# Kernel tuning notes

Measured on AMD Instinct MI355X. Metric: run time of the kernel, lower is better.

Reference implementation:

```python
import jax, jax.numpy as jnp
import numpy as np
from jax.ops import segment_sum

N_NODES = 1_000_000
N_EDGES = 10_000_000


def gcn_conv(x, W, b, src, dst, n_nodes):
    """PyG GCNConv: add self-loops, sym-normalize, linear, scatter-sum, bias."""
    h = x @ W  # [N, out]
    loop = jnp.arange(n_nodes, dtype=src.dtype)
    s = jnp.concatenate([src, loop])  # sources incl. self-loops
    d = jnp.concatenate([dst, loop])  # targets incl. self-loops
    deg = segment_sum(jnp.ones(s.shape[0], dtype=h.dtype), d, num_segments=n_nodes)
    dinv = jnp.where(deg > 0, jax.lax.rsqrt(deg), 0.0)  # deg^-1/2, 0 for isolated
    norm = dinv[s] * dinv[d]  # [E+N]
    msg = h[s] * norm[:, None]  # gather + scale
    out = segment_sum(msg, d, num_segments=n_nodes)  # scatter-add at targets
    return out + b


def setup_inputs() -> dict:
    key = jax.random.key(0)
    k1, k2, k3, k4, k5 = jax.random.split(key, 5)
    x = jax.random.normal(k1, (N_NODES, 3), dtype=jnp.float32)
    edge_index = jax.random.randint(k2, (2, N_EDGES), 0, N_NODES, dtype=jnp.int64)
    # Glorot-ish init for the two GCNConv layers (3->8, 8->2) with bias
    W1 = jax.random.normal(k3, (3, 8), dtype=jnp.float32) * (1.0 / np.sqrt(3.0))
    b1 = jnp.zeros((8,), dtype=jnp.float32)
    W2 = jax.random.normal(k4, (8, 2), dtype=jnp.float32) * (1.0 / np.sqrt(8.0))
    b2 = jnp.zeros((2,), dtype=jnp.float32)
    return {"x": x, "edge_index": edge_index, "W1": W1, "b1": b1, "W2": W2, "b2": b2}


def reference(x, edge_index, W1, b1, W2, b2):
    src, dst = edge_index[0], edge_index[1]
    n = x.shape[0]
    h = gcn_conv(x, W1, b1, src, dst, n)
    h = jax.nn.relu(h)
    return gcn_conv(h, W2, b2, src, dst, n)
```

## Files before the change

kernel.cpp:

```cpp
#include <hip/hip_runtime.h>


#define BSH 12
#define BKT 4096
#define NBKT_MAX 256
#define CAP 43008
#define TILE 8192
#define MSB 512
#define AGB 512

__device__ inline unsigned bf16r(float f) {
    unsigned u = __float_as_uint(f);
    return (u + 0x7FFFu + ((u >> 16) & 1u)) & 0xFFFF0000u;
}

__device__ inline void xq_dec(unsigned u, float& v0, float& v1, float& v2) {
    float sc = __uint_as_float((((u >> 27) & 31u) + 104u) << 23);
    v0 = (float)(((int)(u << 5)) >> 23) * sc;
    v1 = (float)(((int)(u << 14)) >> 23) * sc;
    v2 = (float)(((int)(u << 23)) >> 23) * sc;
}

__global__ void k_init(int* __restrict__ bcur, int nbkt) {
    int t = threadIdx.x;
    if (t < nbkt) bcur[t] = t * CAP;
}

__global__ void k_msplit(const int* __restrict__ src, const int* __restrict__ dst,
                         int* __restrict__ bcur, unsigned* __restrict__ esort, int e) {
    __shared__ unsigned stage[TILE];
    __shared__ unsigned char bid[TILE];
    __shared__ int h[NBKT_MAX];
    __shared__ int lscan[NBKT_MAX];
    __shared__ int baseadj[NBKT_MAX];
    int t = threadIdx.x;
    int base = blockIdx.x * TILE;
    int cnt = min(TILE, e - base);
    if (t < NBKT_MAX) h[t] = 0;
    __syncthreads();

    unsigned val[16];
    int bk[16], rnk[16];
#pragma unroll
    for (int k = 0; k < 16; ++k) {
        int i = base + k * MSB + t;
        bk[k] = -1;
        if (i < e) {
            int d = __builtin_nontemporal_load(&dst[i]);
            int s = __builtin_nontemporal_load(&src[i]);
            bk[k] = d >> BSH;
            val[k] = ((unsigned)(d & (BKT - 1)) << 20) | (unsigned)s;
            rnk[k] = atomicAdd(&h[bk[k]], 1);
        }
    }
    __syncthreads();
    int c = (t < NBKT_MAX) ? h[t] : 0;
    __syncthreads();
    if (t < NBKT_MAX) lscan[t] = c;
    __syncthreads();
    for (int off = 1; off < NBKT_MAX; off <<= 1) {
        int w = (t < NBKT_MAX && t >= off) ? lscan[t - off] : 0;
        __syncthreads();
        if (t < NBKT_MAX) lscan[t] += w;
        __syncthreads();
    }
    int ex = (t < NBKT_MAX) ? (lscan[t] - c) : 0;
    __syncthreads();
    if (t < NBKT_MAX) {
        lscan[t] = ex;
        if (c > 0) baseadj[t] = atomicAdd(&bcur[t], c) - ex;
    }
    __syncthreads();

#pragma unroll
    for (int k = 0; k < 16; ++k) {
        if (bk[k] >= 0) {
            int idx = lscan[bk[k]] + rnk[k];
            stage[idx] = val[k];
            bid[idx] = (unsigned char)bk[k];
        }
    }
    __syncthreads();
#pragma unroll
    for (int k = 0; k < 16; ++k) {
        int j = k * MSB + t;
        if (j < cnt) esort[baseadj[bid[j]] + j] = stage[j];
    }
}

__global__ void k_deg_xd(const unsigned* __restrict__ esort, const int* __restrict__ bcur,
                         const float* __restrict__ x,
                         unsigned* __restrict__ xq, float* __restrict__ dinv, int n) {
    __shared__ int deg[BKT];
    int b = blockIdx.x, t = threadIdx.x;
#pragma unroll
    for (int k = 0; k < BKT / AGB; ++k) deg[k * AGB + t] = 0;
    __syncthreads();
    int beg = b * CAP, end = bcur[b];
    int m = end - beg;
    int ng = (m + 3) >> 2;
    for (int g = t; g < ng; g += AGB) {
        int p = beg + g * 4;
        uint4 v = *(const uint4*)(esort + p);
        int lim = end - p;
        if (lim > 0) atomicAdd(&deg[v.x >> 20], 1);
        if (lim > 1) atomicAdd(&deg[v.y >> 20], 1);
        if (lim > 2) atomicAdd(&deg[v.z >> 20], 1);
        if (lim > 3) atomicAdd(&deg[v.w >> 20], 1);
    }
    __syncthreads();
#pragma unroll
    for (int k = 0; k < BKT / AGB; ++k) {
        int dl = k * AGB + t;
        int node = (b << BSH) + dl;
        if (node >= n) continue;
        float di = rsqrtf((float)deg[dl] + 1.0f);
        float v0 = x[3 * node] * di, v1 = x[3 * node + 1] * di, v2 = x[3 * node + 2] * di;
        dinv[node] = di;
        float mx = fmaxf(fmaxf(fabsf(v0), fabsf(v1)), fabsf(v2));
        int ee;
        frexpf(mx, &ee);
        ee = min(max(ee, -15), 16);
        float sc = exp2f((float)(8 - ee));
        int m0 = min(max(__float2int_rn(v0 * sc), -256), 255);
        int m1 = min(max(__float2int_rn(v1 * sc), -256), 255);
        int m2 = min(max(__float2int_rn(v2 * sc), -256), 255);
        xq[node] = ((unsigned)(ee + 15) << 27) |
                   ((unsigned)(m0 & 0x1FF) << 18) |
                   ((unsigned)(m1 & 0x1FF) << 9) |
                   (unsigned)(m2 & 0x1FF);
    }
}

__global__ void k_l1(const unsigned* __restrict__ esort, const int* __restrict__ bcur,
                     const unsigned* __restrict__ xq, const float* __restrict__ dinv,
                     const float* __restrict__ W1, const float* __restrict__ b1,
                     const float* __restrict__ W2, unsigned* __restrict__ g2, int n) {
    __shared__ float acc[BKT * 3];
    int b = blockIdx.x, t = threadIdx.x;
#pragma unroll
    for (int k = 0; k < BKT * 3 / AGB; ++k) acc[k * AGB + t] = 0.0f;
    __syncthreads();
    int beg = b * CAP, end = bcur[b];
    int m = end - beg;
    int ng = (m + 7) >> 3;
    for (int g = t; g < ng; g += AGB) {
        int p = beg + g * 8;
        uint4 va = *(const uint4*)(esort + p);
        uint4 vb = *(const uint4*)(esort + p + 4);
        unsigned ed[8] = { va.x, va.y, va.z, va.w, vb.x, vb.y, vb.z, vb.w };
        int lim = end - p;
        unsigned u[8];
#pragma unroll
        for (int j = 0; j < 8; ++j)
            u[j] = (j < lim) ? xq[ed[j] & 0xFFFFFu] : 0u;
#pragma unroll
        for (int j = 0; j < 8; ++j) {
            if (j < lim) {
                float s0, s1, s2;
                xq_dec(u[j], s0, s1, s2);
                int q = ed[j] >> 20;
                atomicAdd(&acc[q * 3 + 0], s0);
                atomicAdd(&acc[q * 3 + 1], s1);
                atomicAdd(&acc[q * 3 + 2], s2);
            }
        }
    }
    __syncthreads();
#pragma unroll
    for (int k = 0; k < BKT / AGB; ++k) {
        int dl = k * AGB + t;
        int node = (b << BSH) + dl;
        if (node >= n) continue;
        float s0, s1, s2;
        xq_dec(xq[node], s0, s1, s2);
        float di = dinv[node];
        float a0 = (acc[dl * 3 + 0] + s0) * di;
        float a1 = (acc[dl * 3 + 1] + s1) * di;
        float a2 = (acc[dl * 3 + 2] + s2) * di;
        float h0 = 0.0f, h1 = 0.0f;
#pragma unroll
        for (int j = 0; j < 8; ++j) {
            float r = fmaxf(a0 * W1[j] + a1 * W1[8 + j] + a2 * W1[16 + j] + b1[j], 0.0f);
            h0 += r * W2[2 * j + 0];
            h1 += r * W2[2 * j + 1];
        }
        g2[node] = (bf16r(h0 * di) >> 16) | bf16r(h1 * di);
    }
}

__global__ void k_l2(const unsigned* __restrict__ esort, const int* __restrict__ bcur,
                     const float* __restrict__ dinv, const unsigned* __restrict__ g2,
                     const float* __restrict__ b2, float2* __restrict__ out, int n) {
    __shared__ float acc[BKT * 2];
    int b = blockIdx.x, t = threadIdx.x;
#pragma unroll
    for (int k = 0; k < BKT * 2 / AGB; ++k) acc[k * AGB + t] = 0.0f;
    __syncthreads();
    int beg = b * CAP, end = bcur[b];
    int m = end - beg;
    int ng = (m + 7) >> 3;
    for (int g = t; g < ng; g += AGB) {
        int p = beg + g * 8;
        uint4 va = *(const uint4*)(esort + p);
        uint4 vb = *(const uint4*)(esort + p + 4);
        unsigned ed[8] = { va.x, va.y, va.z, va.w, vb.x, vb.y, vb.z, vb.w };
        int lim = end - p;
        unsigned u[8];
#pragma unroll
        for (int j = 0; j < 8; ++j)
            u[j] = (j < lim) ? g2[ed[j] & 0xFFFFFu] : 0u;
#pragma unroll
        for (int j = 0; j < 8; ++j) {
            if (j < lim) {
                int q = ed[j] >> 20;
                atomicAdd(&acc[q * 2 + 0], __uint_as_float(u[j] << 16));
                atomicAdd(&acc[q * 2 + 1], __uint_as_float(u[j] & 0xFFFF0000u));
            }
        }
    }
    __syncthreads();
#pragma unroll
    for (int k = 0; k < BKT / AGB; ++k) {
        int dl = k * AGB + t;
        int node = (b << BSH) + dl;
        if (node >= n) continue;
        unsigned gg = g2[node];
        float s0 = __uint_as_float(gg << 16);
        float s1 = __uint_as_float(gg & 0xFFFF0000u);
        float di = dinv[node];
        out[node] = make_float2((acc[dl * 2 + 0] + s0) * di + b2[0],
                                (acc[dl * 2 + 1] + s1) * di + b2[1]);
    }
}

extern "C" void kernel_launch(void* const* d_in, const int* in_sizes, int n_in,
                              void* d_out, int out_size, void* d_ws, size_t ws_size,
                              hipStream_t stream) {
    const float* x  = (const float*)d_in[0];
    const int*   ei = (const int*)d_in[1];
    const float* W1 = (const float*)d_in[2];
    const float* b1 = (const float*)d_in[3];
    const float* W2 = (const float*)d_in[4];
    const float* b2 = (const float*)d_in[5];
    float2* out = (float2*)d_out;

    const int n = in_sizes[0] / 3;
    const int e = in_sizes[1] / 2;
    const int* src = ei;
    const int* dst = ei + e;
    const int nbkt = (n + BKT - 1) >> BSH;

    char* w = (char*)d_ws;
    unsigned* xq    = (unsigned*)w;  w += (size_t)n * sizeof(unsigned);
    float*    dinv  = (float*)w;     w += (size_t)n * sizeof(float);
    unsigned* g2    = (unsigned*)w;  w += (size_t)n * sizeof(unsigned);
    unsigned* esort = (unsigned*)w;  w += ((size_t)nbkt * CAP + 64) * sizeof(unsigned);
    int*      bcur  = (int*)w;

    const int nb_ms = (e + TILE - 1) / TILE;

    k_init  <<<1, 256, 0, stream>>>(bcur, nbkt);
    k_msplit<<<nb_ms, MSB, 0, stream>>>(src, dst, bcur, esort, e);
    k_deg_xd<<<nbkt, AGB, 0, stream>>>(esort, bcur, x, xq, dinv, n);
    k_l1    <<<nbkt, AGB, 0, stream>>>(esort, bcur, xq, dinv, W1, b1, W2, g2, n);
    k_l2    <<<nbkt, AGB, 0, stream>>>(esort, bcur, dinv, g2, b2, out, n);
}
```

Measured before the change: 365.4 us.

## Split per-bucket aggregation across two blocks with bf16 partial sums

Each layer's bucket aggregation now runs on twice as many blocks, each handling half of a bucket's edges. Partial sums are written as packed bf16 to a workspace, and a separate finalize kernel combines them. This fills more CUs, since there are only about 245 buckets on a 256-CU part. It also enlarges the msplit tile and block size, and uses nontemporal loads in the degree pass. The cost is two extra launches, extra global traffic for the partials, and further bf16 rounding of the aggregates.

```diff
diff --git a/kernel.cpp b/kernel.cpp
--- a/kernel.cpp
+++ b/kernel.cpp
@@ -5,13 +5,21 @@
 #define BKT 4096
 #define NBKT_MAX 256
 #define CAP 43008
-#define TILE 8192
-#define MSB 512
+#define TILE 16384
+#define MSB 1024
 #define AGB 512
+
+typedef unsigned uvec4 __attribute__((ext_vector_type(4)));
 
 __device__ inline unsigned bf16r(float f) {
     unsigned u = __float_as_uint(f);
     return (u + 0x7FFFu + ((u >> 16) & 1u)) & 0xFFFF0000u;
+}
+__device__ inline unsigned pack2(float a, float b) {
+    return (bf16r(a) >> 16) | (bf16r(b) & 0xFFFF0000u);
+}
+__device__ inline float unp(unsigned w, int half) {
+    return half ? __uint_as_float(w & 0xFFFF0000u) : __uint_as_float(w << 16);
 }
 
 __device__ inline void xq_dec(unsigned u, float& v0, float& v1, float& v2) {
@@ -101,7 +109,7 @@
     int ng = (m + 3) >> 2;
     for (int g = t; g < ng; g += AGB) {
         int p = beg + g * 4;
-        uint4 v = *(const uint4*)(esort + p);
+        uvec4 v = __builtin_nontemporal_load((const uvec4*)(esort + p));
         int lim = end - p;
         if (lim > 0) atomicAdd(&deg[v.x >> 20], 1);
         if (lim > 1) atomicAdd(&deg[v.y >> 20], 1);
@@ -132,24 +140,27 @@
     }
 }
 
-__global__ void k_l1(const unsigned* __restrict__ esort, const int* __restrict__ bcur,
-                     const unsigned* __restrict__ xq, const float* __restrict__ dinv,
-                     const float* __restrict__ W1, const float* __restrict__ b1,
-                     const float* __restrict__ W2, unsigned* __restrict__ g2, int n) {
+__global__ void k_l1a(const unsigned* __restrict__ esort, const int* __restrict__ bcur,
+                      const unsigned* __restrict__ xq, unsigned* __restrict__ part1) {
     __shared__ float acc[BKT * 3];
-    int b = blockIdx.x, t = threadIdx.x;
+    int bid = blockIdx.x, b = bid >> 1, hh = bid & 1;
+    int t = threadIdx.x;
 #pragma unroll
     for (int k = 0; k < BKT * 3 / AGB; ++k) acc[k * AGB + t] = 0.0f;
     __syncthreads();
     int beg = b * CAP, end = bcur[b];
     int m = end - beg;
-    int ng = (m + 7) >> 3;
+    int half = (((m + 1) >> 1) + 7) & ~7;
+    int s0 = beg + hh * half;
+    int e0 = min(end, s0 + half);
+    int mh = e0 - s0;
+    int ng = (mh + 7) >> 3;
     for (int g = t; g < ng; g += AGB) {
-        int p = beg + g * 8;
-        uint4 va = *(const uint4*)(esort + p);
-        uint4 vb = *(const uint4*)(esort + p + 4);
+        int p = s0 + g * 8;
+        uvec4 va = *(const uvec4*)(esort + p);
+        uvec4 vb = *(const uvec4*)(esort + p + 4);
         unsigned ed[8] = { va.x, va.y, va.z, va.w, vb.x, vb.y, vb.z, vb.w };
-        int lim = end - p;
+        int lim = e0 - p;
         unsigned u[8];
 #pragma unroll
         for (int j = 0; j < 8; ++j)
@@ -157,27 +168,46 @@
 #pragma unroll
         for (int j = 0; j < 8; ++j) {
             if (j < lim) {
-                float s0, s1, s2;
-                xq_dec(u[j], s0, s1, s2);
+                float s0f, s1f, s2f;
+                xq_dec(u[j], s0f, s1f, s2f);
                 int q = ed[j] >> 20;
-                atomicAdd(&acc[q * 3 + 0], s0);
-                atomicAdd(&acc[q * 3 + 1], s1);
-                atomicAdd(&acc[q * 3 + 2], s2);
+                atomicAdd(&acc[q * 3 + 0], s0f);
+                atomicAdd(&acc[q * 3 + 1], s1f);
+                atomicAdd(&acc[q * 3 + 2], s2f);
             }
         }
     }
     __syncthreads();
+    unsigned* pb = part1 + (size_t)bid * 6144;
+#pragma unroll
+    for (int j = 0; j < 3; ++j)
+        for (int i = t; i < 2048; i += AGB)
+            pb[j * 2048 + i] = pack2(acc[(2 * i) * 3 + j], acc[(2 * i + 1) * 3 + j]);
+}
+
+__global__ void k_l1b(const unsigned* __restrict__ part1, const unsigned* __restrict__ xq,
+                      const float* __restrict__ dinv,
+                      const float* __restrict__ W1, const float* __restrict__ b1,
+                      const float* __restrict__ W2, unsigned* __restrict__ g2, int n) {
+    int b = blockIdx.x, t = threadIdx.x;
+    const unsigned* pa = part1 + (size_t)(2 * b) * 6144;
+    const unsigned* pbv = part1 + (size_t)(2 * b + 1) * 6144;
 #pragma unroll
     for (int k = 0; k < BKT / AGB; ++k) {
         int dl = k * AGB + t;
         int node = (b << BSH) + dl;
         if (node >= n) continue;
+        int i = dl >> 1, hf = dl & 1;
+        float a[3];
+#pragma unroll
+        for (int j = 0; j < 3; ++j)
+            a[j] = unp(pa[j * 2048 + i], hf) + unp(pbv[j * 2048 + i], hf);
         float s0, s1, s2;
         xq_dec(xq[node], s0, s1, s2);
         float di = dinv[node];
-        float a0 = (acc[dl * 3 + 0] + s0) * di;
-        float a1 = (acc[dl * 3 + 1] + s1) * di;
-        float a2 = (acc[dl * 3 + 2] + s2) * di;
+        float a0 = (a[0] + s0) * di;
+        float a1 = (a[1] + s1) * di;
+        float a2 = (a[2] + s2) * di;
         float h0 = 0.0f, h1 = 0.0f;
 #pragma unroll
         for (int j = 0; j < 8; ++j) {
@@ -189,23 +219,27 @@
     }
 }
 
-__global__ void k_l2(const unsigned* __restrict__ esort, const int* __restrict__ bcur,
-                     const float* __restrict__ dinv, const unsigned* __restrict__ g2,
-                     const float* __restrict__ b2, float2* __restrict__ out, int n) {
+__global__ void k_l2a(const unsigned* __restrict__ esort, const int* __restrict__ bcur,
+                      const unsigned* __restrict__ g2, unsigned* __restrict__ part2) {
     __shared__ float acc[BKT * 2];
-    int b = blockIdx.x, t = threadIdx.x;
+    int bid = blockIdx.x, b = bid >> 1, hh = bid & 1;
+    int t = threadIdx.x;
 #pragma unroll
     for (int k = 0; k < BKT * 2 / AGB; ++k) acc[k * AGB + t] = 0.0f;
     __syncthreads();
     int beg = b * CAP, end = bcur[b];
     int m = end - beg;
-    int ng = (m + 7) >> 3;
+    int half = (((m + 1) >> 1) + 7) & ~7;
+    int s0 = beg + hh * half;
+    int e0 = min(end, s0 + half);
+    int mh = e0 - s0;
+    int ng = (mh + 7) >> 3;
     for (int g = t; g < ng; g += AGB) {
-        int p = beg + g * 8;
-        uint4 va = *(const uint4*)(esort + p);
-        uint4 vb = *(const uint4*)(esort + p + 4);
+        int p = s0 + g * 8;
+        uvec4 va = *(const uvec4*)(esort + p);
+        uvec4 vb = *(const uvec4*)(esort + p + 4);
         unsigned ed[8] = { va.x, va.y, va.z, va.w, vb.x, vb.y, vb.z, vb.w };
-        int lim = end - p;
+        int lim = e0 - p;
         unsigned u[8];
 #pragma unroll
         for (int j = 0; j < 8; ++j)
@@ -220,17 +254,32 @@
         }
     }
     __syncthreads();
+    unsigned* pb = part2 + (size_t)bid * 4096;
+#pragma unroll
+    for (int j = 0; j < 2; ++j)
+        for (int i = t; i < 2048; i += AGB)
+            pb[j * 2048 + i] = pack2(acc[(2 * i) * 2 + j], acc[(2 * i + 1) * 2 + j]);
+}
+
+__global__ void k_l2b(const unsigned* __restrict__ part2, const unsigned* __restrict__ g2,
+                      const float* __restrict__ dinv, const float* __restrict__ b2,
+                      float2* __restrict__ out, int n) {
+    int b = blockIdx.x, t = threadIdx.x;
+    const unsigned* pa = part2 + (size_t)(2 * b) * 4096;
+    const unsigned* pbv = part2 + (size_t)(2 * b + 1) * 4096;
 #pragma unroll
     for (int k = 0; k < BKT / AGB; ++k) {
         int dl = k * AGB + t;
         int node = (b << BSH) + dl;
         if (node >= n) continue;
+        int i = dl >> 1, hf = dl & 1;
+        float a0 = unp(pa[i], hf) + unp(pbv[i], hf);
+        float a1 = unp(pa[2048 + i], hf) + unp(pbv[2048 + i], hf);
         unsigned gg = g2[node];
         float s0 = __uint_as_float(gg << 16);
         float s1 = __uint_as_float(gg & 0xFFFF0000u);
         float di = dinv[node];
-        out[node] = make_float2((acc[dl * 2 + 0] + s0) * di + b2[0],
-                                (acc[dl * 2 + 1] + s1) * di + b2[1]);
+        out[node] = make_float2((a0 + s0) * di + b2[0], (a1 + s1) * di + b2[1]);
     }
 }
 
@@ -256,13 +305,16 @@
     float*    dinv  = (float*)w;     w += (size_t)n * sizeof(float);
     unsigned* g2    = (unsigned*)w;  w += (size_t)n * sizeof(unsigned);
     unsigned* esort = (unsigned*)w;  w += ((size_t)nbkt * CAP + 64) * sizeof(unsigned);
-    int*      bcur  = (int*)w;
+    int*      bcur  = (int*)w;       w += 1024 * sizeof(int);
+    unsigned* part  = (unsigned*)w;
 
     const int nb_ms = (e + TILE - 1) / TILE;
 
     k_init  <<<1, 256, 0, stream>>>(bcur, nbkt);
     k_msplit<<<nb_ms, MSB, 0, stream>>>(src, dst, bcur, esort, e);
     k_deg_xd<<<nbkt, AGB, 0, stream>>>(esort, bcur, x, xq, dinv, n);
-    k_l1    <<<nbkt, AGB, 0, stream>>>(esort, bcur, xq, dinv, W1, b1, W2, g2, n);
-    k_l2    <<<nbkt, AGB, 0, stream>>>(esort, bcur, dinv, g2, b2, out, n);
-}
+    k_l1a   <<<nbkt * 2, AGB, 0, stream>>>(esort, bcur, xq, part);
+    k_l1b   <<<nbkt, AGB, 0, stream>>>(part, xq, dinv, W1, b1, W2, g2, n);
+    k_l2a   <<<nbkt * 2, AGB, 0, stream>>>(esort, bcur, g2, part);
+    k_l2b   <<<nbkt, AGB, 0, stream>>>(part, g2, dinv, b2, out, n);
+}
```

Result: slower. 379.6 us (+3.9%).
